# Optimization experiments

Hardware: AMD Instinct MI355X
Metric: run time of the kernel (lower is better)

## Reference

```python
import jax, jax.numpy as jnp
from jax import lax
import numpy as np

LATENT = 512
LABEL = 128
BATCH = 1024


def _maxpool2(x):
    # 2x2 max pool, stride 2, NCHW
    return lax.reduce_window(x, -jnp.inf, lax.max, (1, 1, 2, 2), (1, 1, 2, 2), 'VALID')


def _encoder(x, c1w, c1b, c2w, c2b, fw, fb):
    dn = ('NCHW', 'OIHW', 'NCHW')
    y = lax.conv_general_dilated(x, c1w, (1, 1), 'SAME', dimension_numbers=dn)
    y = _maxpool2(jax.nn.relu(y + c1b[None, :, None, None]))  # [B,32,14,14]
    y = lax.conv_general_dilated(y, c2w, (1, 1), 'SAME', dimension_numbers=dn)
    y = _maxpool2(jax.nn.relu(y + c2b[None, :, None, None]))  # [B,64,7,7]
    y = y.reshape(y.shape[0], -1)                              # [B,3136]
    return y @ fw.T + fb                                       # [B,latent]


def _hopfield_w(rep):
    # rho = mean over ALL elements (matches torch.mean(x))
    rho = jnp.mean(rep)
    t = rep - rho                      # [label, latent]
    w = t.T @ t                        # sum of rank-1 outer products
    w = w * (1.0 - jnp.eye(w.shape[0], dtype=w.dtype))  # zero diagonal
    return w / LABEL


def _clustering(lat, w):
    # batched fixed-length Hopfield relaxation with min-energy tracking
    s0 = jnp.tanh(lat)                 # [B,L]
    B = s0.shape[0]

    def step(carry, _):
        s, min_e, min_s = carry
        prev = lax.stop_gradient(s)    # torch detaches prev_s each iter
        s_new = jnp.abs(prev) * jnp.sign(prev @ w.T)      # [B,L]
        e = -jnp.einsum('bi,ij,bj->b', s_new, w, s_new)    # [B]
        better = e < min_e
        min_e = jnp.where(better, e, min_e)
        min_s = jnp.where(better[:, None], s_new, min_s)
        return (s_new, min_e, min_s), None

    init = (s0, jnp.full((B,), jnp.inf, dtype=s0.dtype), jnp.zeros_like(s0))
    (_, _, min_s), _ = lax.scan(step, init, None, length=LATENT)
    return min_s


def setup_inputs() -> dict:
    key = jax.random.key(0)
    ks = jax.random.split(key, 11)
    d = {}
    d['image'] = jax.random.normal(ks[0], (BATCH, 1, 28, 28), dtype=jnp.float32)
    d['label_images'] = jax.random.uniform(ks[1], (LABEL, 1, 28, 28), dtype=jnp.float32)
    d['conv1_w'] = jax.random.normal(ks[2], (32, 1, 5, 5), dtype=jnp.float32) * 0.1
    d['conv1_b'] = jnp.zeros((32,), dtype=jnp.float32)
    d['conv2_w'] = jax.random.normal(ks[3], (64, 32, 5, 5), dtype=jnp.float32) * 0.05
    d['conv2_b'] = jnp.zeros((64,), dtype=jnp.float32)
    d['fc1_w'] = jax.random.normal(ks[4], (LATENT, 64 * 7 * 7), dtype=jnp.float32) * 0.02
    d['fc1_b'] = jnp.zeros((LATENT,), dtype=jnp.float32)
    d['fcn_w'] = jax.random.normal(ks[5], (LABEL, LATENT), dtype=jnp.float32) * 0.05
    d['fcn_b'] = jnp.zeros((LABEL,), dtype=jnp.float32)
    return d


def reference(image, label_images, conv1_w, conv1_b, conv2_w, conv2_b,
              fc1_w, fc1_b, fcn_w, fcn_b):
    rep = jnp.tanh(_encoder(label_images, conv1_w, conv1_b, conv2_w, conv2_b, fc1_w, fc1_b))  # [label,L]
    lat = _encoder(image, conv1_w, conv1_b, conv2_w, conv2_b, fc1_w, fc1_b)                    # [B,L]
    # FCN on detached latents (torch: .clone().detach())
    label = jax.nn.softmax(lax.stop_gradient(lat) @ fcn_w.T + fcn_b, axis=1)                   # [B,label]
    w = _hopfield_w(rep)                                                                        # [L,L]
    min_s = _clustering(lat, w)                                                                 # [B,L]
    out = jax.nn.softmax(jnp.abs(min_s @ rep.T), axis=1)                                        # [B,label]
    return (out, label)
```

## Files before the change

kernel.cpp:

```cpp
#include <hip/hip_runtime.h>
#include <hip/hip_bf16.h>
#include <math.h>

#define BATCH 1024
#define LABEL 128
#define LATENT 512
#define NTOT 1152

typedef short short8 __attribute__((ext_vector_type(8)));
typedef float f32x16 __attribute__((ext_vector_type(16)));

__device__ __forceinline__ unsigned short f2bf(float f) {
    __hip_bfloat16 h = __float2bfloat16(f);
    return *(unsigned short*)&h;
}
__device__ __forceinline__ float bf2f(unsigned short u) {
    __hip_bfloat16 h; *(unsigned short*)&h = u;
    return __bfloat162float(h);
}


__global__ __launch_bounds__(256) void conv1_pool(const float* __restrict__ image,
                                                  const float* __restrict__ limg,
                                                  const float* __restrict__ wt,
                                                  const float* __restrict__ bias,
                                                  unsigned short* __restrict__ o1b) {
    const int n = blockIdx.x;
    const float* in = (n < BATCH) ? (image + (size_t)n * 784)
                                  : (limg + (size_t)(n - BATCH) * 784);
    __shared__ float pin[32][32];
    __shared__ float wts[32 * 25];
    const int tid = threadIdx.x;
    unsigned short* ob = o1b + (size_t)n * 12800;
    for (int i = tid; i < 256; i += 256) {
        int pl_ = i >> 7, r = i & 127;
        ob[pl_ * 6400 + 6272 + r] = 0;
    }
    for (int idx = tid; idx < 32 * 32; idx += 256) ((float*)pin)[idx] = 0.f;
    __syncthreads();
    for (int idx = tid; idx < 784; idx += 256) {
        int y = idx / 28, x = idx % 28;
        pin[y + 2][x + 2] = in[idx];
    }
    for (int idx = tid; idx < 800; idx += 256) wts[idx] = wt[idx];
    __syncthreads();
    const int oc = tid & 31;
    float wk[25];
    #pragma unroll
    for (int k = 0; k < 25; ++k) wk[k] = wts[oc * 25 + k];
    float b = bias[oc];
    const int slot_lo = (oc & 7);
    const int gq = oc >> 3;
    for (int o = tid; o < 6272; o += 256) {
        int p = o >> 5, py = p / 14, px = p % 14;
        float win[6][6];
        #pragma unroll
        for (int r = 0; r < 6; ++r)
        #pragma unroll
        for (int c = 0; c < 6; ++c)
            win[r][c] = pin[2 * py + r][2 * px + c];
        float a00 = b, a01 = b, a10 = b, a11 = b;
        #pragma unroll
        for (int ky = 0; ky < 5; ++ky)
        #pragma unroll
        for (int kx = 0; kx < 5; ++kx) {
            float w = wk[ky * 5 + kx];
            a00 = fmaf(win[ky][kx], w, a00);
            a01 = fmaf(win[ky][kx + 1], w, a01);
            a10 = fmaf(win[ky + 1][kx], w, a10);
            a11 = fmaf(win[ky + 1][kx + 1], w, a11);
        }
        float v = fmaxf(fmaxf(fmaxf(a00, a01), fmaxf(a10, a11)), 0.f);
        unsigned short b1 = f2bf(v); float r1 = v - bf2f(b1);
        unsigned short b2 = f2bf(r1);
        int off = p * 32 + (((gq ^ (p >> 1)) & 3) << 3) + slot_lo;
        ob[off] = b1; ob[6400 + off] = b2;
    }
}

__global__ __launch_bounds__(256) void bprep(const float* __restrict__ w,
                                             unsigned short* __restrict__ Bf) {
    int idx = blockIdx.x * 256 + threadIdx.x;
    if (idx >= 102400) return;
    int j = idx & 7, lane = (idx >> 3) & 63, ocT = (idx >> 9) & 1, s = idx >> 10;
    int q = lane >> 5, nn = lane & 31;
    int k = 16 * s + 8 * q + j;
    int tap = k >> 5, ic = k & 31;
    int oc = 32 * ocT + nn;
    float v = w[oc * 800 + ic * 25 + tap];
    unsigned short b1 = f2bf(v);
    unsigned short b2 = f2bf(v - bf2f(b1));
    size_t base = ((size_t)(s * 2 + ocT) * 2) * 512 + lane * 8 + j;
    Bf[base] = b1; Bf[base + 512] = b2;
}

#define BSTR ((size_t)512 * 3136)
#define ASTR ((size_t)NTOT * 3136)
__global__ __launch_bounds__(256) void wprep(const float* __restrict__ w,
                                             unsigned short* __restrict__ B3) {
    int idx = blockIdx.x * 256 + threadIdx.x;
    if (idx >= 512 * 3136) return;
    float v = w[idx];
    unsigned short b1 = f2bf(v);
    float r1 = v - bf2f(b1);
    unsigned short b2 = f2bf(r1);
    unsigned short b3 = f2bf(r1 - bf2f(b2));
    B3[idx] = b1; B3[BSTR + idx] = b2; B3[2 * BSTR + idx] = b3;
}

__global__ __launch_bounds__(256) void conv2_mfma(const unsigned short* __restrict__ o1b,
                                                  const unsigned short* __restrict__ Bf,
                                                  const float* __restrict__ bias,
                                                  unsigned short* __restrict__ out3) {
    const int n = blockIdx.x;
    __shared__ __align__(16) unsigned short pl[12800];
    const int tid = threadIdx.x;
    const int lane = tid & 63, wv = tid >> 6;
    const int ocT = wv & 1, mh = wv >> 1;

    {
        const float4* src = (const float4*)(o1b + (size_t)n * 12800);
        float4* dst = (float4*)pl;
        for (int i = tid; i < 1600; i += 256) dst[i] = src[i];
    }
    __syncthreads();

    const int m_ = lane & 31, q = lane >> 5;
    int ym[4], xm[4], mm[4], tvv[4];
    #pragma unroll
    for (int tt = 0; tt < 4; ++tt) {
        int t = 4 * mh + tt;
        tvv[tt] = (t < 7);
        int m = 32 * t + m_;
        mm[tt] = m;
        ym[tt] = m / 14;
        xm[tt] = m - 14 * ym[tt];
    }
    f32x16 acc[4];
    {
        float bs = bias[32 * ocT + m_];
        #pragma unroll
        for (int tt = 0; tt < 4; ++tt)
        #pragma unroll
        for (int r = 0; r < 16; ++r) acc[tt][r] = bs;
    }

    for (int s = 0; s < 50; ++s) {
        const unsigned short* bp = Bf + ((size_t)(s * 2 + ocT) * 2) * 512 + lane * 8;
        short8 b1 = *(const short8*)(bp);
        short8 b2 = *(const short8*)(bp + 512);
        int kb = 16 * s + 8 * q;
        int tap = kb >> 5, ic0 = kb & 31, g = ic0 >> 3;
        int ky = (tap * 13) >> 6;
        int kx = tap - ky * 5;
        int iyk = ky - 2, ixk = kx - 2;
        int pq2 = iyk * 14 + ixk;
        short8 a1[4], a2[4];
        #pragma unroll
        for (int tt = 0; tt < 4; ++tt) {
            int iy = ym[tt] + iyk, ix = xm[tt] + ixk;
            int valid = tvv[tt] & ((unsigned)iy < 14u) & ((unsigned)ix < 14u);
            int cpt = valid ? (mm[tt] + pq2) : 196;
            int addr = cpt * 32 + (((g ^ (cpt >> 1)) & 3) << 3);
            a1[tt] = *(const short8*)(pl + addr);
            a2[tt] = *(const short8*)(pl + 6400 + addr);
        }
        #pragma unroll
        for (int tt = 0; tt < 4; ++tt)
            acc[tt] = __builtin_amdgcn_mfma_f32_32x32x16_bf16(a1[tt], b1, acc[tt], 0, 0, 0);
        #pragma unroll
        for (int tt = 0; tt < 4; ++tt)
            acc[tt] = __builtin_amdgcn_mfma_f32_32x32x16_bf16(a1[tt], b2, acc[tt], 0, 0, 0);
        #pragma unroll
        for (int tt = 0; tt < 4; ++tt)
            acc[tt] = __builtin_amdgcn_mfma_f32_32x32x16_bf16(a2[tt], b1, acc[tt], 0, 0, 0);
    }
    __syncthreads();

    float* hx = (float*)pl;
    {
        const int oc = 32 * ocT + m_;
        #pragma unroll
        for (int tt = 0; tt < 4; ++tt)
        #pragma unroll
        for (int e = 0; e < 8; ++e) {
            const int reg = 2 * e;
            const int r = (reg & 3) + 8 * (reg >> 2) + 4 * q;
            const int m = 32 * (4 * mh + tt) + r;
            if (m < 196) {
                float xm2 = fmaxf(acc[tt][reg], acc[tt][reg + 1]);
                int y = (m * 2341) >> 15;
                int px = (m - 14 * y) >> 1;
                hx[(y * 7 + px) * 65 + oc] = xm2;
            }
        }
    }
    __syncthreads();

    const size_t OSTR = ASTR;
    for (int idx = tid; idx < 3136; idx += 256) {
        int oc2 = (idx * 2675) >> 17;
        int p = idx - 49 * oc2;
        int py = (p * 9363) >> 16;
        int px = p - 7 * py;
        float v = fmaxf(hx[(2 * py * 7 + px) * 65 + oc2],
                        hx[((2 * py + 1) * 7 + px) * 65 + oc2]);
        v = fmaxf(v, 0.f);
        unsigned short b1 = f2bf(v);
        float r1 = v - bf2f(b1);
        unsigned short b2 = f2bf(r1);
        unsigned short b3 = f2bf(r1 - bf2f(b2));
        size_t o = (size_t)n * 3136 + idx;
        out3[o] = b1; out3[OSTR + o] = b2; out3[2 * OSTR + o] = b3;
    }
}

__global__ __launch_bounds__(256) void fc1_mfma(const unsigned short* __restrict__ A3,
                                                const unsigned short* __restrict__ B3,
                                                float* __restrict__ part) {
    __shared__ unsigned short As[3][2048];
    __shared__ unsigned short Bs[3][2048];
    const int tid = threadIdx.x;
    const int n0 = blockIdx.x * 64, m0 = blockIdx.y * 64;
    const int koff = blockIdx.z * 448;
    const int lr = tid >> 2, g = tid & 3;
    const int slot = (((g ^ (lr >> 1)) & 3) << 3);
    const int lane = tid & 63, wv = tid >> 6;
    const int nq = wv & 1, mq = wv >> 1;
    const int q = lane >> 5, l31 = lane & 31;
    const int rA = 32 * nq + l31, rB = 32 * mq + l31;
    f32x16 acc;
    #pragma unroll
    for (int r = 0; r < 16; ++r) acc[r] = 0.f;

    for (int bk = 0; bk < 448; bk += 32) {
        const size_t ka = (size_t)(koff + bk + (g << 3));
        short8 av[3], bv[3];
        #pragma unroll
        for (int p = 0; p < 3; ++p) {
            av[p] = *(const short8*)(A3 + p * ASTR + (size_t)(n0 + lr) * 3136 + ka);
            bv[p] = *(const short8*)(B3 + p * BSTR + (size_t)(m0 + lr) * 3136 + ka);
        }
        __syncthreads();
        #pragma unroll
        for (int p = 0; p < 3; ++p) {
            *(short8*)&As[p][(lr << 5) + slot] = av[p];
            *(short8*)&Bs[p][(lr << 5) + slot] = bv[p];
        }
        __syncthreads();
        #pragma unroll
        for (int s2 = 0; s2 < 32; s2 += 16) {
            const int gg = (s2 + (q << 3)) >> 3;
            const int sa = (((gg ^ (rA >> 1)) & 3) << 3);
            const int sb = (((gg ^ (rB >> 1)) & 3) << 3);
            short8 a1 = *(const short8*)&As[0][(rA << 5) + sa];
            short8 a2 = *(const short8*)&As[1][(rA << 5) + sa];
            short8 a3 = *(const short8*)&As[2][(rA << 5) + sa];
            short8 b1 = *(const short8*)&Bs[0][(rB << 5) + sb];
            short8 b2 = *(const short8*)&Bs[1][(rB << 5) + sb];
            short8 b3 = *(const short8*)&Bs[2][(rB << 5) + sb];
            acc = __builtin_amdgcn_mfma_f32_32x32x16_bf16(a1, b1, acc, 0, 0, 0);
            acc = __builtin_amdgcn_mfma_f32_32x32x16_bf16(a1, b2, acc, 0, 0, 0);
            acc = __builtin_amdgcn_mfma_f32_32x32x16_bf16(a2, b1, acc, 0, 0, 0);
            acc = __builtin_amdgcn_mfma_f32_32x32x16_bf16(a2, b2, acc, 0, 0, 0);
            acc = __builtin_amdgcn_mfma_f32_32x32x16_bf16(a1, b3, acc, 0, 0, 0);
            acc = __builtin_amdgcn_mfma_f32_32x32x16_bf16(a3, b1, acc, 0, 0, 0);
        }
    }
    float* pb = part + (size_t)blockIdx.z * NTOT * 512;
    #pragma unroll
    for (int reg = 0; reg < 16; ++reg) {
        int nn = n0 + 32 * nq + (reg & 3) + 8 * (reg >> 2) + 4 * q;
        int mmo = m0 + 32 * mq + l31;
        pb[(size_t)nn * 512 + mmo] = acc[reg];
    }
}

__global__ __launch_bounds__(256) void fc1_reduce(const float* __restrict__ part,
                                                  const float* __restrict__ bias,
                                                  float* __restrict__ lat,
                                                  float* __restrict__ rep) {
    int idx = blockIdx.x * 256 + threadIdx.x;
    int m = idx & 511;
    float v = bias[m];
    #pragma unroll
    for (int kz = 0; kz < 7; ++kz) v += part[(size_t)kz * NTOT * 512 + idx];
    if (idx < BATCH * 512) lat[idx] = v;
    else rep[idx - BATCH * 512] = tanhf(v);
}

__global__ __launch_bounds__(128) void fcn_softmax(const float* __restrict__ lat,
                                                   const float* __restrict__ fw,
                                                   const float* __restrict__ fb,
                                                   float* __restrict__ out) {
    const int b = blockIdx.x;
    const int j = threadIdx.x;
    __shared__ float lrow[512];
    __shared__ float red[128];
    for (int i = j; i < 512; i += 128) lrow[i] = lat[b * 512 + i];
    __syncthreads();
    const float4* w4 = (const float4*)(fw + j * 512);
    float acc = fb[j];
    #pragma unroll 4
    for (int qq = 0; qq < 128; ++qq) {
        float4 a = ((const float4*)lrow)[qq];
        float4 w = w4[qq];
        acc += a.x * w.x + a.y * w.y + a.z * w.z + a.w * w.w;
    }
    red[j] = acc;
    __syncthreads();
    for (int off = 64; off >= 1; off >>= 1) {
        if (j < off) red[j] = fmaxf(red[j], red[j + off]);
        __syncthreads();
    }
    float mx = red[0];
    __syncthreads();
    float ex = expf(acc - mx);
    red[j] = ex;
    __syncthreads();
    for (int off = 64; off >= 1; off >>= 1) {
        if (j < off) red[j] += red[j + off];
        __syncthreads();
    }
    out[b * 128 + j] = ex / red[0];
}

__global__ __launch_bounds__(256) void rho_kernel(const float* __restrict__ rep,
                                                  float* __restrict__ rho) {
    __shared__ float red[256];
    const int tid = threadIdx.x;
    float s = 0.f;
    for (int i = tid; i < LABEL * LATENT; i += 256) s += rep[i];
    red[tid] = s;
    __syncthreads();
    for (int off = 128; off >= 1; off >>= 1) {
        if (tid < off) red[tid] += red[tid + off];
        __syncthreads();
    }
    if (tid == 0) rho[0] = red[0] / (float)(LABEL * LATENT);
}

__global__ __launch_bounds__(256) void t_kernel(const float* __restrict__ rep,
                                                const float* __restrict__ rho,
                                                float* __restrict__ tT) {
    int idx = blockIdx.x * 256 + threadIdx.x;
    int i = idx / 128, k = idx % 128;
    tT[idx] = rep[k * 512 + i] - rho[0];
}

__global__ __launch_bounds__(256) void w_kernel(const float* __restrict__ tT,
                                                float* __restrict__ w) {
    int idx = blockIdx.x * 256 + threadIdx.x;
    int i = idx >> 9, j = idx & 511;
    const float4* a = (const float4*)(tT + i * 128);
    const float4* b = (const float4*)(tT + j * 128);
    float acc = 0.f;
    #pragma unroll 8
    for (int q = 0; q < 32; ++q) {
        float4 av = a[q], bv = b[q];
        acc += av.x * bv.x + av.y * bv.y + av.z * bv.z + av.w * bv.w;
    }
    w[idx] = (i == j) ? 0.f : acc * (1.f / 128.f);
}

#define CB 2
__device__ __forceinline__ float sgnf(float x) {
    return (x > 0.f) ? 1.f : ((x < 0.f) ? -1.f : 0.f);
}

__global__ __launch_bounds__(256) void clustering(const float* __restrict__ lat,
                                                  const float* __restrict__ w,
                                                  const float* __restrict__ rep,
                                                  float* __restrict__ out) {
    const int tid = threadIdx.x;
    const int row0 = blockIdx.x * CB;
    __shared__ float sbuf[CB][512];
    __shared__ float mins[CB][512];
    __shared__ float red[256];
    __shared__ float part_e[4][CB];
    __shared__ int part_c[4];
    __shared__ float min_e[CB];
    __shared__ int copyf[CB];
    __shared__ int donef[CB];
    __shared__ int cnt[CB];
    __shared__ int jidx[CB][512];
    __shared__ float jdel[CB][512];
    const int i0 = 2 * tid, i1 = 2 * tid + 1;
    const int wave = tid >> 6, lane = tid & 63;

    float sm10[CB], sm11[CB], sm20[CB], sm21[CB], h0[CB], h1[CB];
    #pragma unroll
    for (int r = 0; r < CB; ++r) {
        float a = tanhf(lat[(row0 + r) * 512 + i0]);
        float b = tanhf(lat[(row0 + r) * 512 + i1]);
        sm10[r] = a; sm11[r] = b;
        sm20[r] = a; sm21[r] = b;
        sbuf[r][i0] = a; sbuf[r][i1] = b;
        h0[r] = 0.f; h1[r] = 0.f;
    }
    if (tid < CB) { min_e[tid] = INFINITY; donef[tid] = 0; cnt[tid] = 0; }
    __syncthreads();

    #pragma unroll 8
    for (int j = 0; j < 512; ++j) {
        float2 wvv = *(const float2*)(w + (size_t)j * 512 + i0);
        #pragma unroll
        for (int r = 0; r < CB; ++r) {
            float sj = sbuf[r][j];
            h0[r] = fmaf(sj, wvv.x, h0[r]);
            h1[r] = fmaf(sj, wvv.y, h1[r]);
        }
    }

    for (int k = 1; k <= 512; ++k) {
        float sn0[CB], sn1[CB];
        int cy = (1 << CB) - 1;
        #pragma unroll
        for (int r = 0; r < CB; ++r) {
            int dn = donef[r];
            if (dn) {
                sn0[r] = sm10[r]; sn1[r] = sm11[r];
            } else {
                sn0[r] = fabsf(sm10[r]) * sgnf(h0[r]);
                sn1[r] = fabsf(sm11[r]) * sgnf(h1[r]);
                if (!(sn0[r] == sm20[r] && sn1[r] == sm21[r])) cy &= ~(1 << r);
                if (sn0[r] != sm10[r]) {
                    int p = atomicAdd(&cnt[r], 1);
                    jidx[r][p] = i0; jdel[r][p] = sn0[r] - sm10[r];
                }
                if (sn1[r] != sm11[r]) {
                    int p = atomicAdd(&cnt[r], 1);
                    jidx[r][p] = i1; jdel[r][p] = sn1[r] - sm11[r];
                }
            }
        }
        #pragma unroll
        for (int m = 32; m >= 1; m >>= 1) cy &= __shfl_xor(cy, m, 64);
        if (lane == 0) part_c[wave] = cy;
        __syncthreads();

        #pragma unroll
        for (int r = 0; r < CB; ++r) {
            const int c = cnt[r];
            #pragma unroll 4
            for (int t = 0; t < c; ++t) {
                const int j = jidx[r][t];
                const float d = jdel[r][t];
                const float2 wvv = *(const float2*)(w + (size_t)j * 512 + i0);
                h0[r] = fmaf(d, wvv.x, h0[r]);
                h1[r] = fmaf(d, wvv.y, h1[r]);
            }
        }
        float ep[CB];
        #pragma unroll
        for (int r = 0; r < CB; ++r) ep[r] = sn0[r] * h0[r] + sn1[r] * h1[r];
        #pragma unroll
        for (int m = 32; m >= 1; m >>= 1) {
            #pragma unroll
            for (int r = 0; r < CB; ++r) ep[r] += __shfl_xor(ep[r], m, 64);
        }
        if (lane == 0) {
            #pragma unroll
            for (int r = 0; r < CB; ++r) part_e[wave][r] = ep[r];
        }
        __syncthreads();

        if (tid < CB) {
            int r = tid;
            if (!donef[r]) {
                float e = -(part_e[0][r] + part_e[1][r] + part_e[2][r] + part_e[3][r]);
                int better = e < min_e[r];
                if (better) min_e[r] = e;
                copyf[r] = better;
                int fl = part_c[0] & part_c[1] & part_c[2] & part_c[3];
                int fixedp = (cnt[r] == 0);
                int cyc = (k >= 2) && ((fl >> r) & 1);
                if (fixedp || cyc) donef[r] = 1;
            } else {
                copyf[r] = 0;
            }
            cnt[r] = 0;
        }
        __syncthreads();

        int alldone = 1;
        #pragma unroll
        for (int r = 0; r < CB; ++r) {
            if (copyf[r]) { mins[r][i0] = sn0[r]; mins[r][i1] = sn1[r]; }
            alldone &= donef[r];
            sm20[r] = sm10[r]; sm21[r] = sm11[r];
            sm10[r] = sn0[r];  sm11[r] = sn1[r];
        }
        if (alldone) break;
    }
    __syncthreads();

    const int j = tid & 127, half = tid >> 7;
    for (int r = 0; r < CB; ++r) {
        const float4* rr = (const float4*)(rep + (size_t)j * 512 + half * 256);
        const float4* ms = (const float4*)(&mins[r][half * 256]);
        float p = 0.f;
        #pragma unroll 8
        for (int q = 0; q < 64; ++q) {
            float4 rv = rr[q], mv = ms[q];
            p += rv.x * mv.x + rv.y * mv.y + rv.z * mv.z + rv.w * mv.w;
        }
        red[tid] = p;
        __syncthreads();
        float v = 0.f;
        if (tid < 128) { v = fabsf(red[tid] + red[tid + 128]); red[tid] = v; }
        __syncthreads();
        for (int off = 64; off >= 1; off >>= 1) {
            if (tid < off) red[tid] = fmaxf(red[tid], red[tid + off]);
            __syncthreads();
        }
        float mx = red[0];
        __syncthreads();
        float ex = 0.f;
        if (tid < 128) { ex = expf(v - mx); red[tid] = ex; }
        __syncthreads();
        for (int off = 64; off >= 1; off >>= 1) {
            if (tid < off) red[tid] += red[tid + off];
            __syncthreads();
        }
        if (tid < 128) out[(size_t)(row0 + r) * 128 + tid] = ex / red[0];
        __syncthreads();
    }
}

extern "C" void kernel_launch(void* const* d_in, const int* in_sizes, int n_in,
                              void* d_out, int out_size, void* d_ws, size_t ws_size,
                              hipStream_t stream) {
    const float* image = (const float*)d_in[0];
    const float* limg  = (const float*)d_in[1];
    const float* c1w   = (const float*)d_in[2];
    const float* c1b   = (const float*)d_in[3];
    const float* c2w   = (const float*)d_in[4];
    const float* c2b   = (const float*)d_in[5];
    const float* f1w   = (const float*)d_in[6];
    const float* f1b   = (const float*)d_in[7];
    const float* fnw   = (const float*)d_in[8];
    const float* fnb   = (const float*)d_in[9];
    float* out = (float*)d_out;
    float* ws  = (float*)d_ws;

    unsigned short* o1b  = (unsigned short*)ws;
    unsigned short* out3 = o1b + (size_t)NTOT * 12800;
    float* lat  = (float*)(out3 + 3 * ASTR);
    float* rep  = lat + (size_t)BATCH * 512;
    float* tT   = rep + (size_t)LABEL * 512;
    float* wmat = tT + (size_t)512 * 128;
    float* rho  = wmat + (size_t)512 * 512;
    unsigned short* Bw3   = (unsigned short*)(rho + 16);
    unsigned short* Bfrag = Bw3 + 3 * BSTR;
    float* part = (float*)ws;

    hipLaunchKernelGGL(bprep, dim3(400), dim3(256), 0, stream, c2w, Bfrag);
    hipLaunchKernelGGL(wprep, dim3(6272), dim3(256), 0, stream, f1w, Bw3);
    hipLaunchKernelGGL(conv1_pool, dim3(NTOT), dim3(256), 0, stream, image, limg, c1w, c1b, o1b);
    hipLaunchKernelGGL(conv2_mfma, dim3(NTOT), dim3(256), 0, stream, o1b, Bfrag, c2b, out3);
    hipLaunchKernelGGL(fc1_mfma, dim3(NTOT / 64, 512 / 64, 7), dim3(256), 0, stream,
                       out3, Bw3, part);
    hipLaunchKernelGGL(fc1_reduce, dim3(NTOT * 512 / 256), dim3(256), 0, stream,
                       part, f1b, lat, rep);
    hipLaunchKernelGGL(fcn_softmax, dim3(BATCH), dim3(128), 0, stream, lat, fnw, fnb,
                       out + (size_t)BATCH * LABEL);
    hipLaunchKernelGGL(rho_kernel, dim3(1), dim3(256), 0, stream, rep, rho);
    hipLaunchKernelGGL(t_kernel, dim3(256), dim3(256), 0, stream, rep, rho, tT);
    hipLaunchKernelGGL(w_kernel, dim3(1024), dim3(256), 0, stream, tT, wmat);
    hipLaunchKernelGGL(clustering, dim3(BATCH / CB), dim3(256), 0, stream, lat, wmat, rep, out);
}
```

Baseline: 426.2 us.

## Use two-term bf16 split for fc1 and precompute initial Hopfield fields via GEMM

```diff
diff --git a/kernel.cpp b/kernel.cpp
--- a/kernel.cpp
+++ b/kernel.cpp
@@ -78,40 +78,38 @@
     }
 }
 
-__global__ __launch_bounds__(256) void bprep(const float* __restrict__ w,
-                                             unsigned short* __restrict__ Bf) {
+#define BSTR ((size_t)512 * 3136)
+#define ASTR ((size_t)NTOT * 3136)
+__global__ __launch_bounds__(256) void prep(const float* __restrict__ c2w,
+                                            const float* __restrict__ f1w,
+                                            unsigned short* __restrict__ Bf,
+                                            unsigned short* __restrict__ Bw2) {
     int idx = blockIdx.x * 256 + threadIdx.x;
-    if (idx >= 102400) return;
-    int j = idx & 7, lane = (idx >> 3) & 63, ocT = (idx >> 9) & 1, s = idx >> 10;
-    int q = lane >> 5, nn = lane & 31;
-    int k = 16 * s + 8 * q + j;
-    int tap = k >> 5, ic = k & 31;
-    int oc = 32 * ocT + nn;
-    float v = w[oc * 800 + ic * 25 + tap];
+    if (idx < 102400) {
+        int j = idx & 7, lane = (idx >> 3) & 63, ocT = (idx >> 9) & 1, s = idx >> 10;
+        int q = lane >> 5, nn = lane & 31;
+        int k = 16 * s + 8 * q + j;
+        int tap = k >> 5, ic = k & 31;
+        int oc = 32 * ocT + nn;
+        float v = c2w[oc * 800 + ic * 25 + tap];
+        unsigned short b1 = f2bf(v);
+        unsigned short b2 = f2bf(v - bf2f(b1));
+        size_t base = ((size_t)(s * 2 + ocT) * 2) * 512 + lane * 8 + j;
+        Bf[base] = b1; Bf[base + 512] = b2;
+        return;
+    }
+    int i2 = idx - 102400;
+    if (i2 >= 512 * 3136) return;
+    float v = f1w[i2];
     unsigned short b1 = f2bf(v);
     unsigned short b2 = f2bf(v - bf2f(b1));
-    size_t base = ((size_t)(s * 2 + ocT) * 2) * 512 + lane * 8 + j;
-    Bf[base] = b1; Bf[base + 512] = b2;
-}
-
-#define BSTR ((size_t)512 * 3136)
-#define ASTR ((size_t)NTOT * 3136)
-__global__ __launch_bounds__(256) void wprep(const float* __restrict__ w,
-                                             unsigned short* __restrict__ B3) {
-    int idx = blockIdx.x * 256 + threadIdx.x;
-    if (idx >= 512 * 3136) return;
-    float v = w[idx];
-    unsigned short b1 = f2bf(v);
-    float r1 = v - bf2f(b1);
-    unsigned short b2 = f2bf(r1);
-    unsigned short b3 = f2bf(r1 - bf2f(b2));
-    B3[idx] = b1; B3[BSTR + idx] = b2; B3[2 * BSTR + idx] = b3;
+    Bw2[i2] = b1; Bw2[BSTR + i2] = b2;
 }
 
 __global__ __launch_bounds__(256) void conv2_mfma(const unsigned short* __restrict__ o1b,
                                                   const unsigned short* __restrict__ Bf,
                                                   const float* __restrict__ bias,
-                                                  unsigned short* __restrict__ out3) {
+                                                  unsigned short* __restrict__ out2) {
     const int n = blockIdx.x;
     __shared__ __align__(16) unsigned short pl[12800];
     const int tid = threadIdx.x;
@@ -197,7 +195,6 @@
     }
     __syncthreads();
 
-    const size_t OSTR = ASTR;
     for (int idx = tid; idx < 3136; idx += 256) {
         int oc2 = (idx * 2675) >> 17;
         int p = idx - 49 * oc2;
@@ -207,19 +204,17 @@
                         hx[((2 * py + 1) * 7 + px) * 65 + oc2]);
         v = fmaxf(v, 0.f);
         unsigned short b1 = f2bf(v);
-        float r1 = v - bf2f(b1);
-        unsigned short b2 = f2bf(r1);
-        unsigned short b3 = f2bf(r1 - bf2f(b2));
+        unsigned short b2 = f2bf(v - bf2f(b1));
         size_t o = (size_t)n * 3136 + idx;
-        out3[o] = b1; out3[OSTR + o] = b2; out3[2 * OSTR + o] = b3;
-    }
-}
-
-__global__ __launch_bounds__(256) void fc1_mfma(const unsigned short* __restrict__ A3,
-                                                const unsigned short* __restrict__ B3,
+        out2[o] = b1; out2[ASTR + o] = b2;
+    }
+}
+
+__global__ __launch_bounds__(256) void fc1_mfma(const unsigned short* __restrict__ A2,
+                                                const unsigned short* __restrict__ B2,
                                                 float* __restrict__ part) {
-    __shared__ unsigned short As[3][2048];
-    __shared__ unsigned short Bs[3][2048];
+    __shared__ unsigned short As[2][2048];
+    __shared__ unsigned short Bs[2][2048];
     const int tid = threadIdx.x;
     const int n0 = blockIdx.x * 64, m0 = blockIdx.y * 64;
     const int koff = blockIdx.z * 448;
@@ -235,15 +230,15 @@
 
     for (int bk = 0; bk < 448; bk += 32) {
         const size_t ka = (size_t)(koff + bk + (g << 3));
-        short8 av[3], bv[3];
-        #pragma unroll
-        for (int p = 0; p < 3; ++p) {
-            av[p] = *(const short8*)(A3 + p * ASTR + (size_t)(n0 + lr) * 3136 + ka);
-            bv[p] = *(const short8*)(B3 + p * BSTR + (size_t)(m0 + lr) * 3136 + ka);
-        }
-        __syncthreads();
-        #pragma unroll
-        for (int p = 0; p < 3; ++p) {
+        short8 av[2], bv[2];
+        #pragma unroll
+        for (int p = 0; p < 2; ++p) {
+            av[p] = *(const short8*)(A2 + p * ASTR + (size_t)(n0 + lr) * 3136 + ka);
+            bv[p] = *(const short8*)(B2 + p * BSTR + (size_t)(m0 + lr) * 3136 + ka);
+        }
+        __syncthreads();
+        #pragma unroll
+        for (int p = 0; p < 2; ++p) {
             *(short8*)&As[p][(lr << 5) + slot] = av[p];
             *(short8*)&Bs[p][(lr << 5) + slot] = bv[p];
         }
@@ -255,16 +250,11 @@
             const int sb = (((gg ^ (rB >> 1)) & 3) << 3);
             short8 a1 = *(const short8*)&As[0][(rA << 5) + sa];
             short8 a2 = *(const short8*)&As[1][(rA << 5) + sa];
-            short8 a3 = *(const short8*)&As[2][(rA << 5) + sa];
             short8 b1 = *(const short8*)&Bs[0][(rB << 5) + sb];
             short8 b2 = *(const short8*)&Bs[1][(rB << 5) + sb];
-            short8 b3 = *(const short8*)&Bs[2][(rB << 5) + sb];
             acc = __builtin_amdgcn_mfma_f32_32x32x16_bf16(a1, b1, acc, 0, 0, 0);
             acc = __builtin_amdgcn_mfma_f32_32x32x16_bf16(a1, b2, acc, 0, 0, 0);
             acc = __builtin_amdgcn_mfma_f32_32x32x16_bf16(a2, b1, acc, 0, 0, 0);
-            acc = __builtin_amdgcn_mfma_f32_32x32x16_bf16(a2, b2, acc, 0, 0, 0);
-            acc = __builtin_amdgcn_mfma_f32_32x32x16_bf16(a1, b3, acc, 0, 0, 0);
-            acc = __builtin_amdgcn_mfma_f32_32x32x16_bf16(a3, b1, acc, 0, 0, 0);
         }
     }
     float* pb = part + (size_t)blockIdx.z * NTOT * 512;
@@ -363,18 +353,57 @@
     w[idx] = (i == j) ? 0.f : acc * (1.f / 128.f);
 }
 
+__global__ __launch_bounds__(256) void hinit(const float* __restrict__ lat,
+                                             const float* __restrict__ w,
+                                             float* __restrict__ hmat) {
+    __shared__ float As[16][68];
+    __shared__ float Bs[16][68];
+    const int tid = threadIdx.x;
+    const int n0 = blockIdx.x * 64, m0 = blockIdx.y * 64;
+    const int lr = tid >> 2;
+    const int lk = (tid & 3) * 4;
+    const int ty = tid >> 4, tx = tid & 15;
+    float c[4][4] = {};
+    for (int k0 = 0; k0 < 512; k0 += 16) {
+        float4 a4 = *(const float4*)(lat + (size_t)(n0 + lr) * 512 + k0 + lk);
+        float4 b4 = *(const float4*)(w + (size_t)(m0 + lr) * 512 + k0 + lk);
+        a4.x = tanhf(a4.x); a4.y = tanhf(a4.y); a4.z = tanhf(a4.z); a4.w = tanhf(a4.w);
+        __syncthreads();
+        As[lk + 0][lr] = a4.x; As[lk + 1][lr] = a4.y; As[lk + 2][lr] = a4.z; As[lk + 3][lr] = a4.w;
+        Bs[lk + 0][lr] = b4.x; Bs[lk + 1][lr] = b4.y; Bs[lk + 2][lr] = b4.z; Bs[lk + 3][lr] = b4.w;
+        __syncthreads();
+        #pragma unroll
+        for (int kk = 0; kk < 16; ++kk) {
+            float av[4], bv[4];
+            #pragma unroll
+            for (int i = 0; i < 4; ++i) av[i] = As[kk][ty * 4 + i];
+            #pragma unroll
+            for (int j = 0; j < 4; ++j) bv[j] = Bs[kk][tx * 4 + j];
+            #pragma unroll
+            for (int i = 0; i < 4; ++i)
+            #pragma unroll
+            for (int j = 0; j < 4; ++j) c[i][j] += av[i] * bv[j];
+        }
+    }
+    #pragma unroll
+    for (int i = 0; i < 4; ++i)
+    #pragma unroll
+    for (int j = 0; j < 4; ++j)
+        hmat[(size_t)(n0 + ty * 4 + i) * 512 + m0 + tx * 4 + j] = c[i][j];
+}
+
 #define CB 2
 __device__ __forceinline__ float sgnf(float x) {
     return (x > 0.f) ? 1.f : ((x < 0.f) ? -1.f : 0.f);
 }
 
 __global__ __launch_bounds__(256) void clustering(const float* __restrict__ lat,
+                                                  const float* __restrict__ hmat,
                                                   const float* __restrict__ w,
                                                   const float* __restrict__ rep,
                                                   float* __restrict__ out) {
     const int tid = threadIdx.x;
     const int row0 = blockIdx.x * CB;
-    __shared__ float sbuf[CB][512];
     __shared__ float mins[CB][512];
     __shared__ float red[256];
     __shared__ float part_e[4][CB];
@@ -395,22 +424,11 @@
         float b = tanhf(lat[(row0 + r) * 512 + i1]);
         sm10[r] = a; sm11[r] = b;
         sm20[r] = a; sm21[r] = b;
-        sbuf[r][i0] = a; sbuf[r][i1] = b;
-        h0[r] = 0.f; h1[r] = 0.f;
+        h0[r] = hmat[(size_t)(row0 + r) * 512 + i0];
+        h1[r] = hmat[(size_t)(row0 + r) * 512 + i1];
     }
     if (tid < CB) { min_e[tid] = INFINITY; donef[tid] = 0; cnt[tid] = 0; }
     __syncthreads();
-
-    #pragma unroll 8
-    for (int j = 0; j < 512; ++j) {
-        float2 wvv = *(const float2*)(w + (size_t)j * 512 + i0);
-        #pragma unroll
-        for (int r = 0; r < CB; ++r) {
-            float sj = sbuf[r][j];
-            h0[r] = fmaf(sj, wvv.x, h0[r]);
-            h1[r] = fmaf(sj, wvv.y, h1[r]);
-        }
-    }
 
     for (int k = 1; k <= 512; ++k) {
         float sn0[CB], sn1[CB];
@@ -545,22 +563,23 @@
     float* ws  = (float*)d_ws;
 
     unsigned short* o1b  = (unsigned short*)ws;
-    unsigned short* out3 = o1b + (size_t)NTOT * 12800;
-    float* lat  = (float*)(out3 + 3 * ASTR);
+    unsigned short* out2 = o1b + (size_t)NTOT * 12800;
+    float* lat  = (float*)(out2 + 2 * ASTR);
     float* rep  = lat + (size_t)BATCH * 512;
     float* tT   = rep + (size_t)LABEL * 512;
     float* wmat = tT + (size_t)512 * 128;
     float* rho  = wmat + (size_t)512 * 512;
-    unsigned short* Bw3   = (unsigned short*)(rho + 16);
-    unsigned short* Bfrag = Bw3 + 3 * BSTR;
+    unsigned short* Bw2   = (unsigned short*)(rho + 16);
+    unsigned short* Bfrag = Bw2 + 2 * BSTR;
+    float* hmat = (float*)(Bfrag + 102400);
     float* part = (float*)ws;
 
-    hipLaunchKernelGGL(bprep, dim3(400), dim3(256), 0, stream, c2w, Bfrag);
-    hipLaunchKernelGGL(wprep, dim3(6272), dim3(256), 0, stream, f1w, Bw3);
+    hipLaunchKernelGGL(prep, dim3((102400 + 512 * 3136 + 255) / 256), dim3(256), 0, stream,
+                       c2w, f1w, Bfrag, Bw2);
     hipLaunchKernelGGL(conv1_pool, dim3(NTOT), dim3(256), 0, stream, image, limg, c1w, c1b, o1b);
-    hipLaunchKernelGGL(conv2_mfma, dim3(NTOT), dim3(256), 0, stream, o1b, Bfrag, c2b, out3);
+    hipLaunchKernelGGL(conv2_mfma, dim3(NTOT), dim3(256), 0, stream, o1b, Bfrag, c2b, out2);
     hipLaunchKernelGGL(fc1_mfma, dim3(NTOT / 64, 512 / 64, 7), dim3(256), 0, stream,
-                       out3, Bw3, part);
+                       out2, Bw2, part);
     hipLaunchKernelGGL(fc1_reduce, dim3(NTOT * 512 / 256), dim3(256), 0, stream,
                        part, f1b, lat, rep);
     hipLaunchKernelGGL(fcn_softmax, dim3(BATCH), dim3(128), 0, stream, lat, fnw, fnb,
@@ -568,5 +587,7 @@
     hipLaunchKernelGGL(rho_kernel, dim3(1), dim3(256), 0, stream, rep, rho);
     hipLaunchKernelGGL(t_kernel, dim3(256), dim3(256), 0, stream, rep, rho, tT);
     hipLaunchKernelGGL(w_kernel, dim3(1024), dim3(256), 0, stream, tT, wmat);
-    hipLaunchKernelGGL(clustering, dim3(BATCH / CB), dim3(256), 0, stream, lat, wmat, rep, out);
-}
+    hipLaunchKernelGGL(hinit, dim3(BATCH / 64, 512 / 64), dim3(256), 0, stream, lat, wmat, hmat);
+    hipLaunchKernelGGL(clustering, dim3(BATCH / CB), dim3(256), 0, stream,
+                       lat, hmat, wmat, rep, out);
+}
```

Result: no change. 422.8 us (-0.8%).
